# Optimization experiments

Hardware: AMD Instinct MI355X
Metric: run time of the kernel (lower is better)

## Reference

```python
import jax, jax.numpy as jnp
import numpy as np

B, T, I, H, L = 256, 256, 256, 1024, 128


def setup_inputs() -> dict:
    key = jax.random.key(0)
    ks = jax.random.split(key, 10)
    s = 0.05
    return {
        "z": jax.random.normal(ks[0], (B, L), dtype=jnp.float32),
        "seq_len": T,
        "target": jax.random.uniform(ks[1], (B, T, I), dtype=jnp.float32),
        "W_z2h": jax.random.normal(ks[2], (H, L), dtype=jnp.float32) * s,
        "b_z2h": jnp.zeros((H,), dtype=jnp.float32),
        "W_ih": jax.random.normal(ks[3], (3 * H, I), dtype=jnp.float32) * s,
        "W_hh": jax.random.normal(ks[4], (3 * H, H), dtype=jnp.float32) * s,
        "b_ih": jnp.zeros((3 * H,), dtype=jnp.float32),
        "b_hh": jnp.zeros((3 * H,), dtype=jnp.float32),
        "W_out": jax.random.normal(ks[5], (I, H), dtype=jnp.float32) * s,
        "b_out": jnp.zeros((I,), dtype=jnp.float32),
    }


def reference(z, seq_len, target, W_z2h, b_z2h, W_ih, W_hh, b_ih, b_hh, W_out, b_out):
    # h0 = tanh(Linear(z))  -- [B, H]
    h0 = jnp.tanh(z @ W_z2h.T + b_z2h)
    # Precompute input-side gate pre-activations for all steps: [T, B, 3H]
    xg = jnp.einsum("bti,gi->tbg", target, W_ih) + b_ih

    hdim = h0.shape[-1]

    def step(h, xg_t):
        hg = h @ W_hh.T + b_hh  # [B, 3H]
        xr, xz, xn = jnp.split(xg_t, 3, axis=-1)
        hr, hz, hn = jnp.split(hg, 3, axis=-1)
        r = jax.nn.sigmoid(xr + hr)
        zg = jax.nn.sigmoid(xz + hz)
        n = jnp.tanh(xn + r * hn)
        h_new = (1.0 - zg) * n + zg * h
        y = jax.nn.sigmoid(h_new @ W_out.T + b_out)  # [B, I]
        return h_new, y

    _, ys = jax.lax.scan(step, h0, xg)  # ys: [T, B, I]
    return jnp.transpose(ys, (1, 0, 2))  # [B, T, I]
```

## Files before the change

### kernel.cpp

```cpp
#include <hip/hip_runtime.h>

#define BB 256
#define TT 256
#define II 256
#define HH 1024
#define LL 128
#define K1 1280
#define GN 3072

#define RP 52
#define GP 20
#define PP 20

typedef short s8v    __attribute__((ext_vector_type(8)));
typedef float f32x4  __attribute__((ext_vector_type(4)));
typedef float f4v    __attribute__((ext_vector_type(4)));
typedef unsigned long long u64;

__device__ __forceinline__ unsigned short f2bf(float f) {
    unsigned u = __float_as_uint(f);
    u += 0x7fffu + ((u >> 16) & 1u);
    return (unsigned short)(u >> 16);
}
__device__ __forceinline__ float bf2f(unsigned short h) {
    return __uint_as_float(((unsigned)h) << 16);
}
__device__ __forceinline__ float sigm(float x) { return 1.0f / (1.0f + __expf(-x)); }

__device__ __forceinline__ s8v cvt8(const float* __restrict__ p) {
    const f4v lo = *(const f4v*)p;
    const f4v hi = *(const f4v*)(p + 4);
    s8v r;
    r[0] = (short)f2bf(lo[0]); r[1] = (short)f2bf(lo[1]);
    r[2] = (short)f2bf(lo[2]); r[3] = (short)f2bf(lo[3]);
    r[4] = (short)f2bf(hi[0]); r[5] = (short)f2bf(hi[1]);
    r[6] = (short)f2bf(hi[2]); r[7] = (short)f2bf(hi[3]);
    return r;
}

__device__ __forceinline__ s8v hload16a(const unsigned short* p) {
    union { u64 q[2]; s8v v; } u;
    u.q[0] = __hip_atomic_load((const u64*)p, __ATOMIC_RELAXED, __HIP_MEMORY_SCOPE_AGENT);
    u.q[1] = __hip_atomic_load((const u64*)p + 1, __ATOMIC_RELAXED, __HIP_MEMORY_SCOPE_AGENT);
    return u.v;
}
template<int FRESH> __device__ __forceinline__ s8v ld16h(const unsigned short* p) {
    if constexpr (FRESH) return *(const s8v*)p;
    else return hload16a(p);
}
template<int FRESH> __device__ __forceinline__ unsigned ld4h(const unsigned short* p) {
    if constexpr (FRESH) return *(const unsigned*)p;
    else return __hip_atomic_load((const unsigned*)p, __ATOMIC_RELAXED, __HIP_MEMORY_SCOPE_AGENT);
}
__device__ __forceinline__ void st4h(unsigned short* p, unsigned v) {
    __hip_atomic_store((unsigned*)p, v, __ATOMIC_RELAXED, __HIP_MEMORY_SCOPE_AGENT);
}

__global__ void k_prep_w(const float* __restrict__ Whh, const float* __restrict__ Wih,
                         unsigned short* __restrict__ Wperm) {
    int o = blockIdx.x;
    int ntt = o / 48, q = o - ntt * 48;
    int gate = q >> 4, j = ntt * 16 + (q & 15);
    int src = gate * HH + j;
    const float* sh = Whh + (size_t)src * HH;
    const float* si = Wih + (size_t)src * II;
    unsigned short* dst = Wperm + (size_t)o * K1;
    for (int k = threadIdx.x; k < K1; k += 256)
        dst[k] = f2bf(k < HH ? sh[k] : si[k - HH]);
}

__global__ void k_prep_misc(const float* __restrict__ bih, const float* __restrict__ bhh,
                            const float* __restrict__ Wout,
                            float* __restrict__ bihp, float* __restrict__ bhhp,
                            unsigned short* __restrict__ Woutb) {
    int idx = blockIdx.x * 256 + threadIdx.x;
    if (idx < GN) {
        int ntt = idx / 48, q = idx - ntt * 48;
        int gate = q >> 4, j = ntt * 16 + (q & 15);
        int src = gate * HH + j;
        bihp[idx] = bih[src];
        bhhp[idx] = bhh[src];
    }
    for (size_t i = (size_t)blockIdx.x * 256 + threadIdx.x; i < (size_t)II * HH;
         i += (size_t)gridDim.x * 256)
        Woutb[i] = f2bf(Wout[i]);
}

__global__ void k_h0(const float* __restrict__ z, const float* __restrict__ Wz,
                     const float* __restrict__ bz, unsigned short* __restrict__ hbuf) {
    int b = blockIdx.x;
    int j0 = threadIdx.x * 4;
    const f4v* zr = (const f4v*)(z + (size_t)b * LL);
    u64 packed = 0;
#pragma unroll
    for (int jj = 0; jj < 4; ++jj) {
        int j = j0 + jj;
        const f4v* wr = (const f4v*)(Wz + (size_t)j * LL);
        float s = bz[j];
#pragma unroll
        for (int i = 0; i < LL / 4; ++i) {
            f4v a = zr[i], w = wr[i];
            s += a[0] * w[0] + a[1] * w[1] + a[2] * w[2] + a[3] * w[3];
        }
        packed |= (u64)f2bf(tanhf(s)) << (16 * jj);
    }
    *(u64*)(hbuf + (size_t)b * HH + j0) = packed;
}

template<int FRESH>
__device__ __forceinline__ void proj_tile(
    const unsigned short* hb, const unsigned short* __restrict__ Woutb,
    float* __restrict__ out, float (*pred)[16 * PP],
    int brow, int io, int wave, int lane, int lr, int lk, int tp, float boutv) {
    f32x4 oa = {0.f, 0.f, 0.f, 0.f};
    const unsigned short* ap = hb + (size_t)(brow + lr) * HH + (wave << 8) + lk;
    const unsigned short* wp = Woutb + (size_t)(io * 16 + lr) * HH + (wave << 8) + lk;
#pragma unroll
    for (int ks = 0; ks < 8; ++ks) {
        s8v a = ld16h<FRESH>(ap + ks * 32);
        s8v w = *(const s8v*)(wp + ks * 32);
        oa = __builtin_amdgcn_mfma_f32_16x16x32_bf16(a, w, oa, 0, 0, 0);
    }
    if (wave >= 1) {
#pragma unroll
        for (int r = 0; r < 4; ++r)
            pred[wave - 1][(((lane >> 4) << 2) + r) * PP + lr] = oa[r];
    }
    __syncthreads();
    if (wave == 0) {
#pragma unroll
        for (int r = 0; r < 4; ++r) {
            int rw = ((lane >> 4) << 2) + r;
            int idx = rw * PP + lr;
            float v = oa[r] + pred[0][idx] + pred[1][idx] + pred[2][idx] + boutv;
            out[(size_t)(brow + rw) * (TT * II) + (size_t)tp * II + io * 16 + lr] = sigm(v);
        }
    }
}

template<int FRESH>
__device__ void run(const float* __restrict__ tgt, const unsigned short* __restrict__ Wperm,
                    const float* __restrict__ bihp, const float* __restrict__ bhhp,
                    unsigned short* hbuf, const unsigned short* __restrict__ Woutb,
                    const float* __restrict__ bout, float* __restrict__ out,
                    unsigned* flags,
                    float (*red)[32 * RP], float* gxn, float (*pred)[16 * PP]) {
    const int tid = threadIdx.x;
    const int wave = tid >> 6, lane = tid & 63;
    const int lr = lane & 15;
    const int lk = (lane >> 4) << 3;
    const int bid = blockIdx.x;
    const int m = bid & 7, nt = bid >> 3;
    const int doproj = (nt < 32);
    const int brow = m * 32 + ((nt >> 4) & 1) * 16;
    const int io = nt & 15;
    const float boutv = bout[io * 16 + lr];

    const int eb = tid & 31, j2 = (tid >> 5) << 1;
    const int ob = nt * 48;
    float bir[2], biz[2], bixn[2], bihn[2];
#pragma unroll
    for (int jj = 0; jj < 2; ++jj) {
        int j = j2 + jj;
        bir[jj]  = bihp[ob + j] + bhhp[ob + j];
        biz[jj]  = bihp[ob + 16 + j] + bhhp[ob + 16 + j];
        bixn[jj] = bihp[ob + 32 + j];
        bihn[jj] = bhhp[ob + 32 + j];
    }

    s8v wreg[30];
    if (wave == 3) {
#pragma unroll
        for (int ks = 0; ks < 2; ++ks)
#pragma unroll
            for (int ni = 0; ni < 3; ++ni)
                wreg[ks * 3 + ni] = *(const s8v*)(Wperm +
                    (size_t)(nt * 48 + ni * 16 + lr) * K1 + 960 + ks * 32 + lk);
#pragma unroll
        for (int ks = 0; ks < 8; ++ks)
#pragma unroll
            for (int ni = 0; ni < 3; ++ni)
                wreg[6 + ks * 3 + ni] = *(const s8v*)(Wperm +
                    (size_t)(nt * 48 + ni * 16 + lr) * K1 + HH + ks * 32 + lk);
    } else {
#pragma unroll
        for (int ks = 0; ks < 10; ++ks)
#pragma unroll
            for (int ni = 0; ni < 3; ++ni)
                wreg[ks * 3 + ni] = *(const s8v*)(Wperm +
                    (size_t)(nt * 48 + ni * 16 + lr) * K1 + wave * 320 + ks * 32 + lk);
    }

    unsigned* gflags = flags + (m << 6);

    for (int t = 0; t < TT; ++t) {
        const unsigned short* hcur = hbuf + (size_t)(FRESH ? t : (t % 3)) * (BB * HH);
        unsigned short* hnxt = hbuf + (size_t)(FRESH ? (t + 1) : ((t + 1) % 3)) * (BB * HH);

        f32x4 acc[6];
#pragma unroll
        for (int i = 0; i < 6; ++i) acc[i] = (f32x4){0.f, 0.f, 0.f, 0.f};
        f32x4 accx[2];
        accx[0] = (f32x4){0.f, 0.f, 0.f, 0.f};
        accx[1] = (f32x4){0.f, 0.f, 0.f, 0.f};

        if (wave == 3) {
#pragma unroll
            for (int cx = 0; cx < 4; ++cx) {
                s8v xa[2][2];
#pragma unroll
                for (int i2 = 0; i2 < 2; ++i2) {
                    int ks = cx * 2 + i2;
#pragma unroll
                    for (int mi = 0; mi < 2; ++mi)
                        xa[i2][mi] = cvt8(tgt +
                            ((size_t)(m * 32 + mi * 16 + lr) * TT + t) * II + ks * 32 + lk);
                }
#pragma unroll
                for (int i2 = 0; i2 < 2; ++i2) {
                    int ks = cx * 2 + i2;
#pragma unroll
                    for (int mi = 0; mi < 2; ++mi) {
                        acc[mi * 3 + 0] = __builtin_amdgcn_mfma_f32_16x16x32_bf16(
                            xa[i2][mi], wreg[6 + ks * 3 + 0], acc[mi * 3 + 0], 0, 0, 0);
                        acc[mi * 3 + 1] = __builtin_amdgcn_mfma_f32_16x16x32_bf16(
                            xa[i2][mi], wreg[6 + ks * 3 + 1], acc[mi * 3 + 1], 0, 0, 0);
                        accx[mi] = __builtin_amdgcn_mfma_f32_16x16x32_bf16(
                            xa[i2][mi], wreg[6 + ks * 3 + 2], accx[mi], 0, 0, 0);
                    }
                }
            }
        }

        if (t > 0 && wave == 0) {
            int guard = 0;
            for (;;) {
                unsigned v = __hip_atomic_load(gflags + lane, __ATOMIC_RELAXED,
                                               __HIP_MEMORY_SCOPE_AGENT);
                if (__ballot(v >= (unsigned)t) == ~0ull) break;
                __builtin_amdgcn_s_sleep(1);
                if (++guard > (1 << 18)) break;
            }
            asm volatile("" ::: "memory");
        }
        __syncthreads();

        if (wave < 3) {
#pragma unroll
            for (int c = 0; c < 2; ++c) {
                s8v a[5][2];
#pragma unroll
                for (int i = 0; i < 5; ++i)
#pragma unroll
                    for (int mi = 0; mi < 2; ++mi)
                        a[i][mi] = ld16h<FRESH>(hcur +
                            (size_t)(m * 32 + mi * 16 + lr) * HH + wave * 320 + (c * 5 + i) * 32 + lk);
#pragma unroll
                for (int i = 0; i < 5; ++i)
#pragma unroll
                    for (int mi = 0; mi < 2; ++mi)
#pragma unroll
                        for (int ni = 0; ni < 3; ++ni)
                            acc[mi * 3 + ni] = __builtin_amdgcn_mfma_f32_16x16x32_bf16(
                                a[i][mi], wreg[(c * 5 + i) * 3 + ni], acc[mi * 3 + ni], 0, 0, 0);
            }
        } else {
            s8v a[2][2];
#pragma unroll
            for (int ks = 0; ks < 2; ++ks)
#pragma unroll
                for (int mi = 0; mi < 2; ++mi)
                    a[ks][mi] = ld16h<FRESH>(hcur +
                        (size_t)(m * 32 + mi * 16 + lr) * HH + 960 + ks * 32 + lk);
#pragma unroll
            for (int ks = 0; ks < 2; ++ks)
#pragma unroll
                for (int mi = 0; mi < 2; ++mi)
#pragma unroll
                    for (int ni = 0; ni < 3; ++ni)
                        acc[mi * 3 + ni] = __builtin_amdgcn_mfma_f32_16x16x32_bf16(
                            a[ks][mi], wreg[ks * 3 + ni], acc[mi * 3 + ni], 0, 0, 0);
#pragma unroll
            for (int mi = 0; mi < 2; ++mi)
#pragma unroll
                for (int r = 0; r < 4; ++r)
                    gxn[(mi * 16 + ((lane >> 4) << 2) + r) * GP + lr] = accx[mi][r];
        }

        if (wave >= 1) {
            float* s = &red[wave - 1][0];
#pragma unroll
            for (int mi = 0; mi < 2; ++mi)
#pragma unroll
                for (int ni = 0; ni < 3; ++ni)
#pragma unroll
                    for (int r = 0; r < 4; ++r)
                        s[(mi * 16 + ((lane >> 4) << 2) + r) * RP + ni * 16 + lr] =
                            acc[mi * 3 + ni][r];
        }
        __syncthreads();
        if (wave == 0) {
#pragma unroll
            for (int mi = 0; mi < 2; ++mi)
#pragma unroll
                for (int ni = 0; ni < 3; ++ni)
#pragma unroll
                    for (int r = 0; r < 4; ++r) {
                        int idx = (mi * 16 + ((lane >> 4) << 2) + r) * RP + ni * 16 + lr;
                        red[0][idx] = acc[mi * 3 + ni][r] + red[0][idx] + red[1][idx] + red[2][idx];
                    }
        }
        __syncthreads();

        {
            const int bg = m * 32 + eb;
            const int jg = nt * 16 + j2;
            unsigned hold = ld4h<FRESH>(hcur + (size_t)bg * HH + jg);
            unsigned packed = 0;
#pragma unroll
            for (int jj = 0; jj < 2; ++jj) {
                int c = j2 + jj;
                float ghr = red[0][eb * RP + c];
                float ghz = red[0][eb * RP + 16 + c];
                float ghn = red[0][eb * RP + 32 + c];
                float gx  = gxn[eb * GP + c];
                float r   = sigm(ghr + bir[jj]);
                float zg  = sigm(ghz + biz[jj]);
                float n   = tanhf(gx + bixn[jj] + r * (ghn + bihn[jj]));
                float ho  = bf2f((unsigned short)(hold >> (16 * jj)));
                packed |= (unsigned)f2bf((1.f - zg) * n + zg * ho) << (16 * jj);
            }
            st4h(hnxt + (size_t)bg * HH + jg, packed);
        }

        asm volatile("s_waitcnt vmcnt(0)" ::: "memory");
        __syncthreads();
        if (tid == 0)
            __hip_atomic_store(gflags + nt, (unsigned)(t + 1), __ATOMIC_RELAXED,
                               __HIP_MEMORY_SCOPE_AGENT);

        if (doproj && t > 0)
            proj_tile<FRESH>(hcur, Woutb, out, pred, brow, io, wave, lane, lr, lk, t - 1, boutv);
    }

    if (doproj) {
        if (wave == 0) {
            int guard = 0;
            for (;;) {
                unsigned v = __hip_atomic_load(gflags + lane, __ATOMIC_RELAXED,
                                               __HIP_MEMORY_SCOPE_AGENT);
                if (__ballot(v >= (unsigned)TT) == ~0ull) break;
                __builtin_amdgcn_s_sleep(1);
                if (++guard > (1 << 18)) break;
            }
            asm volatile("" ::: "memory");
        }
        __syncthreads();
        proj_tile<FRESH>(hbuf + (size_t)(FRESH ? TT : (TT % 3)) * (BB * HH),
                         Woutb, out, pred, brow, io, wave, lane, lr, lk, TT - 1, boutv);
    }
}

__global__ __launch_bounds__(256, 2) void dec_main(
    const float* __restrict__ tgt, const unsigned short* __restrict__ Wperm,
    const float* __restrict__ bihp, const float* __restrict__ bhhp,
    unsigned short* hbuf, const unsigned short* __restrict__ Woutb,
    const float* __restrict__ bout, float* __restrict__ out,
    unsigned* flags, int fresh) {
    __shared__ float red[3][32 * RP];
    __shared__ float gxn[32 * GP];
    __shared__ float pred[3][16 * PP];
    if (fresh)
        run<1>(tgt, Wperm, bihp, bhhp, hbuf, Woutb, bout, out, flags, red, gxn, pred);
    else
        run<0>(tgt, Wperm, bihp, bhhp, hbuf, Woutb, bout, out, flags, red, gxn, pred);
}

extern "C" void kernel_launch(void* const* d_in, const int* in_sizes, int n_in,
                              void* d_out, int out_size, void* d_ws, size_t ws_size,
                              hipStream_t stream) {
    const float* z    = (const float*)d_in[0];
    const float* tgt  = (const float*)d_in[2];
    const float* Wz2h = (const float*)d_in[3];
    const float* bz2h = (const float*)d_in[4];
    const float* Wih  = (const float*)d_in[5];
    const float* Whh  = (const float*)d_in[6];
    const float* bih  = (const float*)d_in[7];
    const float* bhh  = (const float*)d_in[8];
    const float* Wout = (const float*)d_in[9];
    const float* bout = (const float*)d_in[10];
    float* out = (float*)d_out;

    char* ws = (char*)d_ws;
    unsigned short* Wperm = (unsigned short*)ws;
    float* bihp           = (float*)(ws + 7864320);
    float* bhhp           = (float*)(ws + 7876608);
    unsigned short* Woutb = (unsigned short*)(ws + 7888896);
    unsigned* flags       = (unsigned*)(ws + 8413184);
    unsigned short* hbuf  = (unsigned short*)(ws + 8415232);

    const size_t need_big = 8415232ull + 257ull * 524288ull;
    const int fresh = (ws_size >= need_big) ? 1 : 0;

    hipMemsetAsync((void*)flags, 0, 2048, stream);
    hipLaunchKernelGGL(k_prep_w, dim3(GN), dim3(256), 0, stream, Whh, Wih, Wperm);
    hipLaunchKernelGGL(k_prep_misc, dim3(1024), dim3(256), 0, stream, bih, bhh, Wout,
                       bihp, bhhp, Woutb);
    hipLaunchKernelGGL(k_h0, dim3(BB), dim3(256), 0, stream, z, Wz2h, bz2h, hbuf);
    hipLaunchKernelGGL(dec_main, dim3(512), dim3(256), 0, stream,
                       tgt, Wperm, bihp, bhhp, hbuf, Woutb, bout, out, flags, fresh);
}
```

Baseline: 5.168 ms.

## Halve persistent grid, widen batch tile, and use fine-grained per-chunk flag polling

```diff
diff --git a/kernel.cpp b/kernel.cpp
--- a/kernel.cpp
+++ b/kernel.cpp
@@ -8,8 +8,8 @@
 #define K1 1280
 #define GN 3072
 
-#define RP 52
-#define GP 20
+#define RP 49
+#define GP 17
 #define PP 20
 
 typedef short s8v    __attribute__((ext_vector_type(8)));
@@ -48,12 +48,45 @@
     if constexpr (FRESH) return *(const s8v*)p;
     else return hload16a(p);
 }
-template<int FRESH> __device__ __forceinline__ unsigned ld4h(const unsigned short* p) {
-    if constexpr (FRESH) return *(const unsigned*)p;
-    else return __hip_atomic_load((const unsigned*)p, __ATOMIC_RELAXED, __HIP_MEMORY_SCOPE_AGENT);
-}
-__device__ __forceinline__ void st4h(unsigned short* p, unsigned v) {
-    __hip_atomic_store((unsigned*)p, v, __ATOMIC_RELAXED, __HIP_MEMORY_SCOPE_AGENT);
+template<int FRESH> __device__ __forceinline__ u64 ld8h(const unsigned short* p) {
+    if constexpr (FRESH) return *(const u64*)p;
+    else return __hip_atomic_load((const u64*)p, __ATOMIC_RELAXED, __HIP_MEMORY_SCOPE_AGENT);
+}
+__device__ __forceinline__ void st8h(unsigned short* p, u64 v) {
+    __hip_atomic_store((u64*)p, v, __ATOMIC_RELAXED, __HIP_MEMORY_SCOPE_AGENT);
+}
+
+__device__ __forceinline__ void poll_pair(const unsigned* p, unsigned t) {
+    if (t == 0) return;
+    int guard = 0;
+    for (;;) {
+        u64 v = __hip_atomic_load((const u64*)p, __ATOMIC_RELAXED, __HIP_MEMORY_SCOPE_AGENT);
+        if ((unsigned)v >= t && (unsigned)(v >> 32) >= t) return;
+        __builtin_amdgcn_s_sleep(1);
+        if (++guard > (1 << 17)) return;
+    }
+}
+__device__ __forceinline__ void poll_range16(const unsigned* p0, int lr, unsigned t) {
+    if (t == 0) return;
+    int guard = 0;
+    for (;;) {
+        unsigned v = __hip_atomic_load(p0 + lr, __ATOMIC_RELAXED, __HIP_MEMORY_SCOPE_AGENT);
+        if (__ballot(v >= t) == ~0ull) break;
+        __builtin_amdgcn_s_sleep(1);
+        if (++guard > (1 << 17)) break;
+    }
+    asm volatile("" ::: "memory");
+}
+__device__ __forceinline__ void poll_range64(const unsigned* p0, int lane, unsigned t) {
+    if (t == 0) return;
+    int guard = 0;
+    for (;;) {
+        unsigned v = __hip_atomic_load(p0 + lane, __ATOMIC_RELAXED, __HIP_MEMORY_SCOPE_AGENT);
+        if (__ballot(v >= t) == ~0ull) break;
+        __builtin_amdgcn_s_sleep(1);
+        if (++guard > (1 << 17)) break;
+    }
+    asm volatile("" ::: "memory");
 }
 
 __global__ void k_prep_w(const float* __restrict__ Whh, const float* __restrict__ Wih,
@@ -136,6 +169,7 @@
             out[(size_t)(brow + rw) * (TT * II) + (size_t)tp * II + io * 16 + lr] = sigm(v);
         }
     }
+    __syncthreads();
 }
 
 template<int FRESH>
@@ -144,24 +178,24 @@
                     unsigned short* hbuf, const unsigned short* __restrict__ Woutb,
                     const float* __restrict__ bout, float* __restrict__ out,
                     unsigned* flags,
-                    float (*red)[32 * RP], float* gxn, float (*pred)[16 * PP]) {
+                    float (*red)[64 * RP], float* gxn, float (*pred)[16 * PP]) {
     const int tid = threadIdx.x;
     const int wave = tid >> 6, lane = tid & 63;
     const int lr = lane & 15;
     const int lk = (lane >> 4) << 3;
     const int bid = blockIdx.x;
-    const int m = bid & 7, nt = bid >> 3;
-    const int doproj = (nt < 32);
-    const int brow = m * 32 + ((nt >> 4) & 1) * 16;
+    const int m = bid >> 6, nt = bid & 63;
+    const int brow = m * 64 + (nt >> 4) * 16;
     const int io = nt & 15;
     const float boutv = bout[io * 16 + lr];
 
-    const int eb = tid & 31, j2 = (tid >> 5) << 1;
+    const int eb = lane;
+    const int j4 = wave << 2;
     const int ob = nt * 48;
-    float bir[2], biz[2], bixn[2], bihn[2];
-#pragma unroll
-    for (int jj = 0; jj < 2; ++jj) {
-        int j = j2 + jj;
+    float bir[4], biz[4], bixn[4], bihn[4];
+#pragma unroll
+    for (int jj = 0; jj < 4; ++jj) {
+        int j = j4 + jj;
         bir[jj]  = bihp[ob + j] + bhhp[ob + j];
         biz[jj]  = bihp[ob + 16 + j] + bhhp[ob + 16 + j];
         bixn[jj] = bihp[ob + 32 + j];
@@ -197,100 +231,84 @@
         const unsigned short* hcur = hbuf + (size_t)(FRESH ? t : (t % 3)) * (BB * HH);
         unsigned short* hnxt = hbuf + (size_t)(FRESH ? (t + 1) : ((t + 1) % 3)) * (BB * HH);
 
-        f32x4 acc[6];
-#pragma unroll
-        for (int i = 0; i < 6; ++i) acc[i] = (f32x4){0.f, 0.f, 0.f, 0.f};
-        f32x4 accx[2];
-        accx[0] = (f32x4){0.f, 0.f, 0.f, 0.f};
-        accx[1] = (f32x4){0.f, 0.f, 0.f, 0.f};
+        f32x4 acc[12];
+#pragma unroll
+        for (int i = 0; i < 12; ++i) acc[i] = (f32x4){0.f, 0.f, 0.f, 0.f};
+        f32x4 accx[4];
+#pragma unroll
+        for (int i = 0; i < 4; ++i) accx[i] = (f32x4){0.f, 0.f, 0.f, 0.f};
 
         if (wave == 3) {
 #pragma unroll
-            for (int cx = 0; cx < 4; ++cx) {
-                s8v xa[2][2];
-#pragma unroll
-                for (int i2 = 0; i2 < 2; ++i2) {
-                    int ks = cx * 2 + i2;
-#pragma unroll
-                    for (int mi = 0; mi < 2; ++mi)
-                        xa[i2][mi] = cvt8(tgt +
-                            ((size_t)(m * 32 + mi * 16 + lr) * TT + t) * II + ks * 32 + lk);
-                }
-#pragma unroll
-                for (int i2 = 0; i2 < 2; ++i2) {
-                    int ks = cx * 2 + i2;
-#pragma unroll
-                    for (int mi = 0; mi < 2; ++mi) {
-                        acc[mi * 3 + 0] = __builtin_amdgcn_mfma_f32_16x16x32_bf16(
-                            xa[i2][mi], wreg[6 + ks * 3 + 0], acc[mi * 3 + 0], 0, 0, 0);
-                        acc[mi * 3 + 1] = __builtin_amdgcn_mfma_f32_16x16x32_bf16(
-                            xa[i2][mi], wreg[6 + ks * 3 + 1], acc[mi * 3 + 1], 0, 0, 0);
-                        accx[mi] = __builtin_amdgcn_mfma_f32_16x16x32_bf16(
-                            xa[i2][mi], wreg[6 + ks * 3 + 2], accx[mi], 0, 0, 0);
-                    }
+            for (int ks = 0; ks < 8; ++ks) {
+                s8v xa[4];
+#pragma unroll
+                for (int mi = 0; mi < 4; ++mi)
+                    xa[mi] = cvt8(tgt +
+                        ((size_t)(m * 64 + mi * 16 + lr) * TT + t) * II + ks * 32 + lk);
+#pragma unroll
+                for (int mi = 0; mi < 4; ++mi) {
+                    acc[mi * 3 + 0] = __builtin_amdgcn_mfma_f32_16x16x32_bf16(
+                        xa[mi], wreg[6 + ks * 3 + 0], acc[mi * 3 + 0], 0, 0, 0);
+                    acc[mi * 3 + 1] = __builtin_amdgcn_mfma_f32_16x16x32_bf16(
+                        xa[mi], wreg[6 + ks * 3 + 1], acc[mi * 3 + 1], 0, 0, 0);
+                    accx[mi] = __builtin_amdgcn_mfma_f32_16x16x32_bf16(
+                        xa[mi], wreg[6 + ks * 3 + 2], accx[mi], 0, 0, 0);
                 }
             }
         }
 
-        if (t > 0 && wave == 0) {
-            int guard = 0;
-            for (;;) {
-                unsigned v = __hip_atomic_load(gflags + lane, __ATOMIC_RELAXED,
-                                               __HIP_MEMORY_SCOPE_AGENT);
-                if (__ballot(v >= (unsigned)t) == ~0ull) break;
-                __builtin_amdgcn_s_sleep(1);
-                if (++guard > (1 << 18)) break;
-            }
-            asm volatile("" ::: "memory");
-        }
-        __syncthreads();
+        if constexpr (!FRESH) {
+            if (wave == 0) poll_range64(gflags, lane, (unsigned)t);
+            __syncthreads();
+        }
 
         if (wave < 3) {
-#pragma unroll
-            for (int c = 0; c < 2; ++c) {
-                s8v a[5][2];
-#pragma unroll
-                for (int i = 0; i < 5; ++i)
-#pragma unroll
-                    for (int mi = 0; mi < 2; ++mi)
-                        a[i][mi] = ld16h<FRESH>(hcur +
-                            (size_t)(m * 32 + mi * 16 + lr) * HH + wave * 320 + (c * 5 + i) * 32 + lk);
-#pragma unroll
-                for (int i = 0; i < 5; ++i)
-#pragma unroll
-                    for (int mi = 0; mi < 2; ++mi)
-#pragma unroll
-                        for (int ni = 0; ni < 3; ++ni)
-                            acc[mi * 3 + ni] = __builtin_amdgcn_mfma_f32_16x16x32_bf16(
-                                a[i][mi], wreg[(c * 5 + i) * 3 + ni], acc[mi * 3 + ni], 0, 0, 0);
+            const unsigned* fp = gflags + wave * 20;
+            poll_pair(fp, (unsigned)t);
+#pragma unroll
+            for (int ci = 0; ci < 10; ++ci) {
+                s8v a[4];
+#pragma unroll
+                for (int mi = 0; mi < 4; ++mi)
+                    a[mi] = ld16h<FRESH>(hcur +
+                        (size_t)(m * 64 + mi * 16 + lr) * HH + wave * 320 + ci * 32 + lk);
+                if (ci < 9) poll_pair(fp + 2 * (ci + 1), (unsigned)t);
+#pragma unroll
+                for (int mi = 0; mi < 4; ++mi)
+#pragma unroll
+                    for (int ni = 0; ni < 3; ++ni)
+                        acc[mi * 3 + ni] = __builtin_amdgcn_mfma_f32_16x16x32_bf16(
+                            a[mi], wreg[ci * 3 + ni], acc[mi * 3 + ni], 0, 0, 0);
             }
         } else {
-            s8v a[2][2];
-#pragma unroll
-            for (int ks = 0; ks < 2; ++ks)
-#pragma unroll
-                for (int mi = 0; mi < 2; ++mi)
-                    a[ks][mi] = ld16h<FRESH>(hcur +
-                        (size_t)(m * 32 + mi * 16 + lr) * HH + 960 + ks * 32 + lk);
-#pragma unroll
-            for (int ks = 0; ks < 2; ++ks)
-#pragma unroll
-                for (int mi = 0; mi < 2; ++mi)
+            poll_pair(gflags + 60, (unsigned)t);
+#pragma unroll
+            for (int ks = 0; ks < 2; ++ks) {
+                s8v a[4];
+#pragma unroll
+                for (int mi = 0; mi < 4; ++mi)
+                    a[mi] = ld16h<FRESH>(hcur +
+                        (size_t)(m * 64 + mi * 16 + lr) * HH + 960 + ks * 32 + lk);
+                if (ks == 0) poll_pair(gflags + 62, (unsigned)t);
+#pragma unroll
+                for (int mi = 0; mi < 4; ++mi)
 #pragma unroll
                     for (int ni = 0; ni < 3; ++ni)
                         acc[mi * 3 + ni] = __builtin_amdgcn_mfma_f32_16x16x32_bf16(
-                            a[ks][mi], wreg[ks * 3 + ni], acc[mi * 3 + ni], 0, 0, 0);
-#pragma unroll
-            for (int mi = 0; mi < 2; ++mi)
+                            a[mi], wreg[ks * 3 + ni], acc[mi * 3 + ni], 0, 0, 0);
+            }
+#pragma unroll
+            for (int mi = 0; mi < 4; ++mi)
 #pragma unroll
                 for (int r = 0; r < 4; ++r)
                     gxn[(mi * 16 + ((lane >> 4) << 2) + r) * GP + lr] = accx[mi][r];
         }
 
-        if (wave >= 1) {
-            float* s = &red[wave - 1][0];
-#pragma unroll
-            for (int mi = 0; mi < 2; ++mi)
+        {
+            float* s = &red[wave][0];
+#pragma unroll
+            for (int mi = 0; mi < 4; ++mi)
 #pragma unroll
                 for (int ni = 0; ni < 3; ++ni)
 #pragma unroll
@@ -299,38 +317,27 @@
                             acc[mi * 3 + ni][r];
         }
         __syncthreads();
-        if (wave == 0) {
-#pragma unroll
-            for (int mi = 0; mi < 2; ++mi)
-#pragma unroll
-                for (int ni = 0; ni < 3; ++ni)
-#pragma unroll
-                    for (int r = 0; r < 4; ++r) {
-                        int idx = (mi * 16 + ((lane >> 4) << 2) + r) * RP + ni * 16 + lr;
-                        red[0][idx] = acc[mi * 3 + ni][r] + red[0][idx] + red[1][idx] + red[2][idx];
-                    }
-        }
-        __syncthreads();
 
         {
-            const int bg = m * 32 + eb;
-            const int jg = nt * 16 + j2;
-            unsigned hold = ld4h<FRESH>(hcur + (size_t)bg * HH + jg);
-            unsigned packed = 0;
-#pragma unroll
-            for (int jj = 0; jj < 2; ++jj) {
-                int c = j2 + jj;
-                float ghr = red[0][eb * RP + c];
-                float ghz = red[0][eb * RP + 16 + c];
-                float ghn = red[0][eb * RP + 32 + c];
+            const int bg = m * 64 + eb;
+            const int jg = nt * 16 + j4;
+            u64 hold8 = ld8h<FRESH>(hcur + (size_t)bg * HH + jg);
+            u64 packed = 0;
+#pragma unroll
+            for (int jj = 0; jj < 4; ++jj) {
+                int c = j4 + jj;
+                int i0 = eb * RP + c;
+                float ghr = red[0][i0] + red[1][i0] + red[2][i0] + red[3][i0];
+                float ghz = red[0][i0 + 16] + red[1][i0 + 16] + red[2][i0 + 16] + red[3][i0 + 16];
+                float ghn = red[0][i0 + 32] + red[1][i0 + 32] + red[2][i0 + 32] + red[3][i0 + 32];
                 float gx  = gxn[eb * GP + c];
                 float r   = sigm(ghr + bir[jj]);
                 float zg  = sigm(ghz + biz[jj]);
                 float n   = tanhf(gx + bixn[jj] + r * (ghn + bihn[jj]));
-                float ho  = bf2f((unsigned short)(hold >> (16 * jj)));
-                packed |= (unsigned)f2bf((1.f - zg) * n + zg * ho) << (16 * jj);
+                float ho  = bf2f((unsigned short)(hold8 >> (16 * jj)));
+                packed |= (u64)f2bf((1.f - zg) * n + zg * ho) << (16 * jj);
             }
-            st4h(hnxt + (size_t)bg * HH + jg, packed);
+            st8h(hnxt + (size_t)bg * HH + jg, packed);
         }
 
         asm volatile("s_waitcnt vmcnt(0)" ::: "memory");
@@ -339,36 +346,26 @@
             __hip_atomic_store(gflags + nt, (unsigned)(t + 1), __ATOMIC_RELAXED,
                                __HIP_MEMORY_SCOPE_AGENT);
 
-        if (doproj && t > 0)
-            proj_tile<FRESH>(hcur, Woutb, out, pred, brow, io, wave, lane, lr, lk, t - 1, boutv);
-    }
-
-    if (doproj) {
-        if (wave == 0) {
-            int guard = 0;
-            for (;;) {
-                unsigned v = __hip_atomic_load(gflags + lane, __ATOMIC_RELAXED,
-                                               __HIP_MEMORY_SCOPE_AGENT);
-                if (__ballot(v >= (unsigned)TT) == ~0ull) break;
-                __builtin_amdgcn_s_sleep(1);
-                if (++guard > (1 << 18)) break;
-            }
-            asm volatile("" ::: "memory");
-        }
-        __syncthreads();
-        proj_tile<FRESH>(hbuf + (size_t)(FRESH ? TT : (TT % 3)) * (BB * HH),
-                         Woutb, out, pred, brow, io, wave, lane, lr, lk, TT - 1, boutv);
-    }
-}
-
-__global__ __launch_bounds__(256, 2) void dec_main(
+        if (t > 0) {
+            poll_range16(gflags + (wave << 4), lr, (unsigned)t);
+            proj_tile<FRESH>(hcur, Woutb, out, pred, brow, io, wave, lane, lr, lk,
+                             t - 1, boutv);
+        }
+    }
+
+    poll_range16(gflags + (wave << 4), lr, (unsigned)TT);
+    proj_tile<FRESH>(hbuf + (size_t)(FRESH ? TT : (TT % 3)) * (BB * HH),
+                     Woutb, out, pred, brow, io, wave, lane, lr, lk, TT - 1, boutv);
+}
+
+__global__ __launch_bounds__(256, 1) void dec_main(
     const float* __restrict__ tgt, const unsigned short* __restrict__ Wperm,
     const float* __restrict__ bihp, const float* __restrict__ bhhp,
     unsigned short* hbuf, const unsigned short* __restrict__ Woutb,
     const float* __restrict__ bout, float* __restrict__ out,
     unsigned* flags, int fresh) {
-    __shared__ float red[3][32 * RP];
-    __shared__ float gxn[32 * GP];
+    __shared__ float red[4][64 * RP];
+    __shared__ float gxn[64 * GP];
     __shared__ float pred[3][16 * PP];
     if (fresh)
         run<1>(tgt, Wperm, bihp, bhhp, hbuf, Woutb, bout, out, flags, red, gxn, pred);
@@ -402,11 +399,11 @@
     const size_t need_big = 8415232ull + 257ull * 524288ull;
     const int fresh = (ws_size >= need_big) ? 1 : 0;
 
-    hipMemsetAsync((void*)flags, 0, 2048, stream);
+    hipMemsetAsync((void*)flags, 0, 1024, stream);
     hipLaunchKernelGGL(k_prep_w, dim3(GN), dim3(256), 0, stream, Whh, Wih, Wperm);
     hipLaunchKernelGGL(k_prep_misc, dim3(1024), dim3(256), 0, stream, bih, bhh, Wout,
                        bihp, bhhp, Woutb);
     hipLaunchKernelGGL(k_h0, dim3(BB), dim3(256), 0, stream, z, Wz2h, bz2h, hbuf);
-    hipLaunchKernelGGL(dec_main, dim3(512), dim3(256), 0, stream,
+    hipLaunchKernelGGL(dec_main, dim3(256), dim3(256), 0, stream,
                        tgt, Wperm, bihp, bhhp, hbuf, Woutb, bout, out, flags, fresh);
 }
```

After: 5.542 ms. 1.07x slower.
